# Kernel optimization log

Measured on AMD Instinct MI355X. Metric: run time of the kernel, lower is better.

Reference implementation:

```python
import math
import jax, jax.numpy as jnp
import numpy as np

B, T_IN, R = 32, 24, 512
T_HIST, WIDTH, MODES, NLAYERS = 24, 128, 64, 4
IN_CH = T_HIST + 4
STEPS = 12
DT = 1.0


def setup_inputs() -> dict:
    key = jax.random.key(0)
    ks = jax.random.split(key, 12)
    scale = 1.0 / math.sqrt(WIDTH * WIDTH)
    return {
        "z": jax.random.normal(ks[0], (B, T_IN, R), dtype=jnp.float32),
        "t_grid": jax.random.uniform(ks[1], (B, T_IN), dtype=jnp.float32) * 100.0,
        "fc0_w": jax.random.normal(ks[2], (IN_CH, WIDTH), dtype=jnp.float32) / math.sqrt(IN_CH),
        "fc0_b": jax.random.normal(ks[3], (WIDTH,), dtype=jnp.float32) * 0.01,
        "spec_wr": jax.random.normal(ks[4], (NLAYERS, WIDTH, WIDTH, MODES), dtype=jnp.float32) * scale,
        "spec_wi": jax.random.normal(ks[5], (NLAYERS, WIDTH, WIDTH, MODES), dtype=jnp.float32) * scale,
        "conv_w": jax.random.normal(ks[6], (NLAYERS, WIDTH, WIDTH), dtype=jnp.float32) / math.sqrt(WIDTH),
        "conv_b": jax.random.normal(ks[7], (NLAYERS, WIDTH), dtype=jnp.float32) * 0.01,
        "fc1_w": jax.random.normal(ks[8], (WIDTH, 2 * WIDTH), dtype=jnp.float32) / math.sqrt(WIDTH),
        "fc1_b": jax.random.normal(ks[9], (2 * WIDTH,), dtype=jnp.float32) * 0.01,
        "fc2_w": jax.random.normal(ks[10], (2 * WIDTH, 1), dtype=jnp.float32) / math.sqrt(2 * WIDTH),
        "fc2_b": jax.random.normal(ks[11], (1,), dtype=jnp.float32) * 0.01,
        "steps": STEPS,
    }


def _fno_block(h, w_cplx, cw, cb, r):
    # h: (B, W, R). Spectral conv: rfft -> truncated complex mul -> irfft.
    x_ft = jnp.fft.rfft(h, axis=-1)                      # (B, W, R//2+1) complex
    m = w_cplx.shape[-1]                                  # modes (<= R//2+1)
    out_m = jnp.einsum('bim,iom->bom', x_ft[:, :, :m], w_cplx)
    out_ft = jnp.pad(out_m, ((0, 0), (0, 0), (0, x_ft.shape[-1] - m)))
    spec = jnp.fft.irfft(out_ft, n=r, axis=-1)
    # 1x1 conv (pointwise over channels) + bias
    pw = jnp.einsum('oi,bir->bor', cw, h) + cb[None, :, None]
    return jax.nn.gelu(spec + pw, approximate=False)


def reference(z, t_grid, fc0_w, fc0_b, spec_wr, spec_wi, conv_w, conv_b,
              fc1_w, fc1_b, fc2_w, fc2_b, steps):
    b, _, r = z.shape
    t_hist = fc0_w.shape[0] - 4
    seq0 = z[:, -t_hist:]                 # (B, t_hist, R)
    t_start = t_grid[:, -1]               # (B,)
    x_coord = jnp.linspace(0.0, 1.0, r, dtype=z.dtype)  # (R,)
    spec_w = spec_wr + 1j * spec_wi       # (L, W, W, M) complex
    nlayers = conv_w.shape[0]

    def step(seq, i):
        tt = t_start + (i + 1).astype(z.dtype) * DT      # (B,)
        ang24 = 2.0 * math.pi * tt / 24.0
        ang168 = 2.0 * math.pi * tt / 168.0
        tf = jnp.stack([
            jnp.broadcast_to(jnp.sin(ang24)[:, None], (b, r)),
            jnp.broadcast_to(jnp.cos(ang24)[:, None], (b, r)),
            jnp.broadcast_to(jnp.sin(ang168)[:, None], (b, r)),
            jnp.broadcast_to(x_coord[None, :], (b, r)),
        ], axis=-1)                                       # (B, R, 4)
        h = jnp.concatenate([jnp.swapaxes(seq, 1, 2), tf], axis=-1)  # (B, R, t_hist+4)
        h = h @ fc0_w + fc0_b                             # (B, R, W)
        h = jnp.swapaxes(h, 1, 2)                         # (B, W, R)
        for l in range(nlayers):
            h = _fno_block(h, spec_w[l], conv_w[l], conv_b[l], r)
        h = jnp.swapaxes(h, 1, 2)                         # (B, R, W)
        h = jax.nn.gelu(h @ fc1_w + fc1_b, approximate=False)
        dx = (h @ fc2_w + fc2_b)[..., 0]                  # (B, R)
        z_next = seq[:, -1, :] + dx
        new_seq = jnp.concatenate([seq[:, 1:], z_next[:, None]], axis=1)
        return new_seq, z_next

    _, preds = jax.lax.scan(step, seq0, jnp.arange(steps))
    return jnp.swapaxes(preds, 0, 1)                      # (B, steps, R)
```

## Files before the change

kernel.cpp:

```cpp
#include <hip/hip_runtime.h>
#include <math.h>


#define NB 32
#define NR 512
#define NW 128
#define NM 64
#define NTH 24
#define NLAY 4
#define NSTEPS 12
#define SEQROWS 36

typedef unsigned short u16;
typedef unsigned int u32;
typedef __attribute__((ext_vector_type(8))) short bf16x8;
typedef __attribute__((ext_vector_type(4))) float f32x4;
#define MFMA16(a, b, c) __builtin_amdgcn_mfma_f32_16x16x32_bf16((a), (b), (c), 0, 0, 0)

__device__ __forceinline__ float gelu_exact(float x) {
    return 0.5f * x * (1.0f + erff(x * 0.70710678118654752f));
}
__device__ __forceinline__ float bf2f(u16 u) {
    union { u32 i; float f; } v; v.i = ((u32)u) << 16; return v.f;
}
__device__ __forceinline__ u16 f2bf_hi(float x) {
    union { float f; u32 i; } v; v.f = x; return (u16)(v.i >> 16);
}
__device__ __forceinline__ u16 f2bf_lo(float x) {
    float h = bf2f(f2bf_hi(x));
    return f2bf_hi(x - h);
}
__device__ __forceinline__ bf16x8 negbf(bf16x8 a) {
#pragma unroll
    for (int i = 0; i < 8; i++) a[i] ^= (short)0x8000;
    return a;
}

__global__ void build_tables_planes(u16* __restrict__ f1, u16* __restrict__ f2,
                                    u16* __restrict__ gt1, u16* __restrict__ gt2) {
    int idx = blockIdx.x * 256 + threadIdx.x;
    int mc = idx >> 9, r = idx & 511, m = mc & 63;
    int p = (m * r) & 511;
    float a = (float)p * (1.0f / 256.0f);
    float c = cospif(a), s = sinpif(a);
    float Fv = (mc < 64) ? c : -s;
    float cm = (m == 0) ? (1.0f / 512.0f) : (2.0f / 512.0f);
    float Gv = (mc < 64) ? cm * c : ((m == 0) ? 0.0f : -cm * s);
    f1[idx] = f2bf_hi(Fv); f2[idx] = f2bf_lo(Fv);
    size_t g = (size_t)r * 128 + mc;
    gt1[g] = f2bf_hi(Gv); gt2[g] = f2bf_lo(Gv);
}

__global__ __launch_bounds__(256) void prep_specw(const float* __restrict__ wr, const float* __restrict__ wi,
                           u16* __restrict__ wr1, u16* __restrict__ wr2,
                           u16* __restrict__ wi1, u16* __restrict__ wi2) {
    __shared__ float tile[128][65];
    int l = blockIdx.x >> 7, o = blockIdx.x & 127;
    int tid = threadIdx.x;
    size_t sbase = (size_t)l * 1048576 + (size_t)o * 64;
    size_t dbase = (size_t)l * 64 * 16384 + (size_t)o * 128;
    for (int pass = 0; pass < 2; pass++) {
        const float* src = pass ? wi : wr;
        u16* d1 = pass ? wi1 : wr1;
        u16* d2 = pass ? wi2 : wr2;
        if (pass) __syncthreads();
        for (int e = tid; e < 8192; e += 256) {
            int i = e >> 6, m = e & 63;
            tile[i][m] = src[sbase + (size_t)i * 8192 + m];
        }
        __syncthreads();
        for (int e = tid; e < 4096; e += 256) {
            int m = e >> 6, i2 = (e & 63) * 2;
            float v0 = tile[i2][m], v1 = tile[i2 + 1][m];
            u32 hh = (u32)f2bf_hi(v0) | ((u32)f2bf_hi(v1) << 16);
            u32 ll = (u32)f2bf_lo(v0) | ((u32)f2bf_lo(v1) << 16);
            size_t d = dbase + (size_t)m * 16384 + i2;
            *(u32*)&d1[d] = hh;
            *(u32*)&d2[d] = ll;
        }
    }
}

__global__ void prep_cw(const float* __restrict__ cw, u16* __restrict__ c1, u16* __restrict__ c2) {
    int idx = blockIdx.x * 256 + threadIdx.x;
    float v = cw[idx];
    c1[idx] = f2bf_hi(v); c2[idx] = f2bf_lo(v);
}

__global__ void prep_fc1t(const float* __restrict__ fc1_w,
                          u16* __restrict__ f11, u16* __restrict__ f12) {
    int idx = blockIdx.x * 256 + threadIdx.x;
    int j = idx >> 7, c = idx & 127;
    float v = fc1_w[(size_t)c * 256 + j];
    f11[idx] = f2bf_hi(v); f12[idx] = f2bf_lo(v);
}

__global__ void init_seq_kernel(const float* __restrict__ z, float* __restrict__ seq) {
    int idx = blockIdx.x * 256 + threadIdx.x;
    int b = idx / (NTH * NR);
    int rem = idx - b * (NTH * NR);
    seq[(size_t)b * SEQROWS * NR + rem] = z[idx];
}

__global__ __launch_bounds__(256) void fc0_kernel(const float* __restrict__ seq,
        const float* __restrict__ t_grid, const float* __restrict__ fc0_w,
        const float* __restrict__ fc0_b, u16* __restrict__ ht1, u16* __restrict__ ht2,
        u16* __restrict__ htc1, u16* __restrict__ htc2, int step) {
    __shared__ float wlds[28 * 128];
    __shared__ float blds[128];
    int b = blockIdx.y, rblk = blockIdx.x;
    int tid = threadIdx.x;
    for (int t = tid; t < 28 * 128; t += 256) wlds[t] = fc0_w[t];
    if (tid < 128) blds[tid] = fc0_b[tid];
    __syncthreads();
    int lane = tid & 63, wq = tid >> 6;
    int r = rblk * 64 + lane;
    float sv[24];
    const float* sp = seq + ((size_t)b * SEQROWS + step) * NR + r;
#pragma unroll
    for (int t = 0; t < 24; t++) sv[t] = sp[(size_t)t * NR];
    float tt = t_grid[b * 24 + 23] + (float)(step + 1);
    float ang24 = 6.28318530717958647692f * tt * (1.0f / 24.0f);
    float ang168 = 6.28318530717958647692f * tt * (1.0f / 168.0f);
    float s24 = sinf(ang24), c24 = cosf(ang24), s168 = sinf(ang168);
    float xc = (float)r * (1.0f / 511.0f);
    size_t rowoff = ((size_t)b * NR + r) * NW;
#pragma unroll 2
    for (int w0 = 0; w0 < 32; w0 += 2) {
        float acc2[2];
#pragma unroll
        for (int q = 0; q < 2; q++) {
            int w = wq * 32 + w0 + q;
            float acc = blds[w];
#pragma unroll
            for (int t = 0; t < 24; t++) acc += sv[t] * wlds[t * 128 + w];
            acc += s24 * wlds[24 * 128 + w] + c24 * wlds[25 * 128 + w]
                 + s168 * wlds[26 * 128 + w] + xc * wlds[27 * 128 + w];
            acc2[q] = acc;
        }
        u16 h0 = f2bf_hi(acc2[0]), h1 = f2bf_hi(acc2[1]);
        u16 l0 = f2bf_lo(acc2[0]), l1 = f2bf_lo(acc2[1]);
        size_t off = rowoff + wq * 32 + w0;
        *(u32*)&ht1[off] = (u32)h0 | ((u32)h1 << 16);
        *(u32*)&ht2[off] = (u32)l0 | ((u32)l1 << 16);
        int w = wq * 32 + w0;
        size_t coff = ((size_t)b * 128 + w) * 512 + r;
        htc1[coff] = h0; htc1[coff + 512] = h1;
        htc2[coff] = l0; htc2[coff + 512] = l1;
    }
}

__global__ __launch_bounds__(256) void dft_mfma(const u16* __restrict__ f1, const u16* __restrict__ f2,
        const u16* __restrict__ htc1, const u16* __restrict__ htc2,
        u16* __restrict__ x1, u16* __restrict__ x2) {
    __shared__ __align__(16) u16 A1[2][32 * 72], A2[2][32 * 72];
    __shared__ __align__(16) u16 B1[2][32 * 72], B2[2][32 * 72];
    int bx = blockIdx.x;
    int mct = blockIdx.y * 32;
    int tid = threadIdx.x, wid = tid >> 6, l = tid & 63;
    int wm0 = (wid >> 1) * 16, wn0 = (wid & 1) * 16;
    int arow = l & 15, kgrp = (l >> 4) * 8;
    f32x4 acc = {0.f, 0.f, 0.f, 0.f};
    int pl = tid >> 7, row = (tid >> 2) & 31, sp = (tid & 3) * 16;
    const u16* asrc = (pl ? f2 : f1) + (size_t)(mct + row) * 512 + sp;
    const u16* bsrc = (pl ? htc2 : htc1)
                      + ((size_t)(bx >> 2) * 128 + (bx & 3) * 32 + row) * 512 + sp;
    int loff = row * 72 + sp;
    u16* ad0 = (pl ? A2[0] : A1[0]) + loff;  u16* ad1 = (pl ? A2[1] : A1[1]) + loff;
    u16* bd0 = (pl ? B2[0] : B1[0]) + loff;  u16* bd1 = (pl ? B2[1] : B1[1]) + loff;
    uint4 oA0, oA1, oB0, oB1, eA0, eA1, eB0, eB1;
    oA0 = *(const uint4*)(asrc);     oA1 = *(const uint4*)(asrc + 8);
    oB0 = *(const uint4*)(bsrc);     oB1 = *(const uint4*)(bsrc + 8);
    *(uint4*)ad0 = oA0; *(uint4*)(ad0 + 8) = oA1;
    *(uint4*)bd0 = oB0; *(uint4*)(bd0 + 8) = oB1;
    oA0 = *(const uint4*)(asrc + 64);  oA1 = *(const uint4*)(asrc + 72);
    oB0 = *(const uint4*)(bsrc + 64);  oB1 = *(const uint4*)(bsrc + 72);
    eA0 = *(const uint4*)(asrc + 128); eA1 = *(const uint4*)(asrc + 136);
    eB0 = *(const uint4*)(bsrc + 128); eB1 = *(const uint4*)(bsrc + 136);
    __syncthreads();
#define DFT_COMPUTE(BUF)                                                       \
    { _Pragma("unroll")                                                        \
      for (int kk = 0; kk < 64; kk += 32) {                                    \
        bf16x8 a1 = *(const bf16x8*)&A1[BUF][(wm0 + arow) * 72 + kk + kgrp];   \
        bf16x8 a2 = *(const bf16x8*)&A2[BUF][(wm0 + arow) * 72 + kk + kgrp];   \
        bf16x8 b1 = *(const bf16x8*)&B1[BUF][(wn0 + arow) * 72 + kk + kgrp];   \
        bf16x8 b2 = *(const bf16x8*)&B2[BUF][(wn0 + arow) * 72 + kk + kgrp];   \
        acc = MFMA16(a1, b1, acc);                                             \
        acc = MFMA16(a1, b2, acc);                                             \
        acc = MFMA16(a2, b1, acc);                                             \
      } }
    for (int k = 0; k < 8; k += 2) {
        DFT_COMPUTE(0)
        *(uint4*)ad1 = oA0; *(uint4*)(ad1 + 8) = oA1;
        *(uint4*)bd1 = oB0; *(uint4*)(bd1 + 8) = oB1;
        if (k < 5) {
            int ko = (k + 3) * 64;
            oA0 = *(const uint4*)(asrc + ko);      oA1 = *(const uint4*)(asrc + ko + 8);
            oB0 = *(const uint4*)(bsrc + ko);      oB1 = *(const uint4*)(bsrc + ko + 8);
        }
        __syncthreads();
        DFT_COMPUTE(1)
        if (k < 6) {
            *(uint4*)ad0 = eA0; *(uint4*)(ad0 + 8) = eA1;
            *(uint4*)bd0 = eB0; *(uint4*)(bd0 + 8) = eB1;
            if (k < 4) {
                int ko = (k + 4) * 64;
                eA0 = *(const uint4*)(asrc + ko);  eA1 = *(const uint4*)(asrc + ko + 8);
                eB0 = *(const uint4*)(bsrc + ko);  eB1 = *(const uint4*)(bsrc + ko + 8);
            }
        }
        __syncthreads();
    }
#undef DFT_COMPUTE
    int mcr = mct + wm0 + (l >> 4) * 4;
    int n0 = bx * 32 + wn0 + (l & 15);
#pragma unroll
    for (int j = 0; j < 4; j++) {
        size_t o0 = (size_t)(mcr + j) * 4096 + n0;
        x1[o0] = f2bf_hi(acc[j]); x2[o0] = f2bf_lo(acc[j]);
    }
}

__global__ __launch_bounds__(256) void modemix_mfma(const u16* __restrict__ x1, const u16* __restrict__ x2,
        const u16* __restrict__ wr1, const u16* __restrict__ wr2,
        const u16* __restrict__ wi1, const u16* __restrict__ wi2,
        u16* __restrict__ y1, u16* __restrict__ y2, int layer) {
    __shared__ __align__(16) u16 POOL[8 * 32 * 136];
    int m = blockIdx.x, oq = blockIdx.y;
    int tid = threadIdx.x, wid = tid >> 6, l = tid & 63;
    int wo0 = (wid >> 1) * 16, wb0 = (wid & 1) * 16;
    int arow = l & 15, kgrp = (l >> 4) * 8;
    size_t wbase = (((size_t)layer * 64 + m) * 128 + oq * 32) * 128;
#pragma unroll
    for (int q = 0; q < 16; q++) {
        const int slab = q >> 1;
        int rr = ((q & 1) << 4) + (tid >> 4);
        int seg = tid & 15;
        const u16* src;
        if      (slab == 0) src = wr1 + wbase + (size_t)rr * 128 + seg * 8;
        else if (slab == 1) src = wr2 + wbase + (size_t)rr * 128 + seg * 8;
        else if (slab == 2) src = wi1 + wbase + (size_t)rr * 128 + seg * 8;
        else if (slab == 3) src = wi2 + wbase + (size_t)rr * 128 + seg * 8;
        else if (slab == 4) src = x1 + (size_t)m * 4096 + rr * 128 + seg * 8;
        else if (slab == 5) src = x2 + (size_t)m * 4096 + rr * 128 + seg * 8;
        else if (slab == 6) src = x1 + (size_t)(64 + m) * 4096 + rr * 128 + seg * 8;
        else                src = x2 + (size_t)(64 + m) * 4096 + rr * 128 + seg * 8;
        *(uint4*)&POOL[slab * 4352 + rr * 136 + seg * 8] = *(const uint4*)src;
    }
    __syncthreads();
    f32x4 ar = {0.f, 0.f, 0.f, 0.f}, ai = {0.f, 0.f, 0.f, 0.f};
    int aoB = (wo0 + arow) * 136 + kgrp;
    int boB = (wb0 + arow) * 136 + kgrp;
#pragma unroll
    for (int kg = 0; kg < 4; kg++) {
        int ao = aoB + kg * 32;
        int bo = boB + kg * 32;
        bf16x8 Wr1 = *(const bf16x8*)&POOL[0 * 4352 + ao];
        bf16x8 Wr2 = *(const bf16x8*)&POOL[1 * 4352 + ao];
        bf16x8 Wi1 = *(const bf16x8*)&POOL[2 * 4352 + ao];
        bf16x8 Wi2 = *(const bf16x8*)&POOL[3 * 4352 + ao];
        bf16x8 Xr1 = *(const bf16x8*)&POOL[4 * 4352 + bo];
        bf16x8 Xr2 = *(const bf16x8*)&POOL[5 * 4352 + bo];
        bf16x8 Xi1 = *(const bf16x8*)&POOL[6 * 4352 + bo];
        bf16x8 Xi2 = *(const bf16x8*)&POOL[7 * 4352 + bo];
        bf16x8 nWi1 = negbf(Wi1), nWi2 = negbf(Wi2);
        ar = MFMA16(Wr1, Xr1, ar); ar = MFMA16(Wr1, Xr2, ar); ar = MFMA16(Wr2, Xr1, ar);
        ar = MFMA16(nWi1, Xi1, ar); ar = MFMA16(nWi1, Xi2, ar); ar = MFMA16(nWi2, Xi1, ar);
        ai = MFMA16(Wi1, Xr1, ai); ai = MFMA16(Wi1, Xr2, ai); ai = MFMA16(Wi2, Xr1, ai);
        ai = MFMA16(Wr1, Xi1, ai); ai = MFMA16(Wr1, Xi2, ai); ai = MFMA16(Wr2, Xi1, ai);
    }
    int ob = oq * 32 + wo0 + (l >> 4) * 4;
    int bb = wb0 + (l & 15);
#pragma unroll
    for (int j = 0; j < 4; j++) {
        size_t o = ((size_t)bb * 128 + ob + j) * 128;
        y1[o + m] = f2bf_hi(ar[j]); y2[o + m] = f2bf_lo(ar[j]);
        y1[o + 64 + m] = f2bf_hi(ai[j]); y2[o + 64 + m] = f2bf_lo(ai[j]);
    }
}

__global__ __launch_bounds__(256) void idft_conv_mfma(const u16* __restrict__ y1, const u16* __restrict__ y2,
        const u16* __restrict__ gt1, const u16* __restrict__ gt2,
        const u16* __restrict__ hc1, const u16* __restrict__ hc2,
        const u16* __restrict__ cw1, const u16* __restrict__ cw2,
        const float* __restrict__ conv_b,
        u16* __restrict__ hn1, u16* __restrict__ hn2,
        u16* __restrict__ htc1, u16* __restrict__ htc2, int layer, int wtr) {
    __shared__ __align__(16) u16 A1[2][2560], A2[2][2560];
    __shared__ __align__(16) u16 B1[2][2560], B2[2][2560];
    __shared__ __align__(16) u16 T1[64 * 66], T2[64 * 66];
    int rt = blockIdx.x * 64, ot = blockIdx.y * 64, b = blockIdx.z;
    int tid = threadIdx.x, wid = tid >> 6, l = tid & 63;
    int wo0 = (wid >> 1) * 32, wr0 = (wid & 1) * 32;
    int arow = (l & 15), kgrp = (l >> 4) * 8;
    int srow = (tid >> 2) & 63, sseg = tid & 3;
    int soff = srow * 40 + sseg * 8;
    const u16* ya = y1 + ((size_t)b * 128 + ot + srow) * 128 + sseg * 8;
    const u16* yb = y2 + ((size_t)b * 128 + ot + srow) * 128 + sseg * 8;
    const u16* ca = cw1 + ((size_t)layer * 128 + ot + srow) * 128 + sseg * 8;
    const u16* cb = cw2 + ((size_t)layer * 128 + ot + srow) * 128 + sseg * 8;
    const u16* ga = gt1 + (size_t)(rt + srow) * 128 + sseg * 8;
    const u16* gb = gt2 + (size_t)(rt + srow) * 128 + sseg * 8;
    const u16* ha = hc1 + ((size_t)b * 512 + rt + srow) * 128 + sseg * 8;
    const u16* hb = hc2 + ((size_t)b * 512 + rt + srow) * 128 + sseg * 8;
    f32x4 acc[2][2] = {{{0.f,0.f,0.f,0.f},{0.f,0.f,0.f,0.f}},{{0.f,0.f,0.f,0.f},{0.f,0.f,0.f,0.f}}};
    uint4 raO0, raO1, rbO0, rbO1, raE0, raE1, rbE0, rbE1;
#define IDFT_LOAD(chk, Ra0, Ra1, Rb0, Rb1)                                    \
    {   int k0_ = ((chk) & 3) * 32;                                           \
        if ((chk) < 4) {                                                      \
            Ra0 = *(const uint4*)(ya + k0_); Ra1 = *(const uint4*)(yb + k0_); \
            Rb0 = *(const uint4*)(ga + k0_); Rb1 = *(const uint4*)(gb + k0_); \
        } else {                                                              \
            Ra0 = *(const uint4*)(ca + k0_); Ra1 = *(const uint4*)(cb + k0_); \
            Rb0 = *(const uint4*)(ha + k0_); Rb1 = *(const uint4*)(hb + k0_); \
        } }
#define IDFT_STORE(BUF, Ra0, Ra1, Rb0, Rb1)                                   \
    {   *(uint4*)(A1[BUF] + soff) = Ra0; *(uint4*)(A2[BUF] + soff) = Ra1;     \
        *(uint4*)(B1[BUF] + soff) = Rb0; *(uint4*)(B2[BUF] + soff) = Rb1; }
#define IDFT_COMPUTE(BUF)                                                     \
    {   bf16x8 bfr[2][2];                                                     \
        _Pragma("unroll")                                                     \
        for (int rf = 0; rf < 2; rf++) {                                      \
            bfr[rf][0] = *(const bf16x8*)&B1[BUF][(wr0 + rf * 16 + arow) * 40 + kgrp]; \
            bfr[rf][1] = *(const bf16x8*)&B2[BUF][(wr0 + rf * 16 + arow) * 40 + kgrp]; \
        }                                                                     \
        _Pragma("unroll")                                                     \
        for (int of = 0; of < 2; of++) {                                      \
            bf16x8 a1 = *(const bf16x8*)&A1[BUF][(wo0 + of * 16 + arow) * 40 + kgrp]; \
            bf16x8 a2 = *(const bf16x8*)&A2[BUF][(wo0 + of * 16 + arow) * 40 + kgrp]; \
            _Pragma("unroll")                                                 \
            for (int rf = 0; rf < 2; rf++) {                                  \
                acc[of][rf] = MFMA16(a1, bfr[rf][0], acc[of][rf]);            \
                acc[of][rf] = MFMA16(a1, bfr[rf][1], acc[of][rf]);            \
                acc[of][rf] = MFMA16(a2, bfr[rf][0], acc[of][rf]);            \
            }                                                                 \
        } }
    IDFT_LOAD(0, raO0, raO1, rbO0, rbO1)
    IDFT_STORE(0, raO0, raO1, rbO0, rbO1)
    IDFT_LOAD(1, raO0, raO1, rbO0, rbO1)
    IDFT_LOAD(2, raE0, raE1, rbE0, rbE1)
    __syncthreads();
    for (int k = 0; k < 8; k += 2) {
        IDFT_COMPUTE(0)
        IDFT_STORE(1, raO0, raO1, rbO0, rbO1)
        if (k < 5) IDFT_LOAD(k + 3, raO0, raO1, rbO0, rbO1)
        __syncthreads();
        IDFT_COMPUTE(1)
        if (k < 6) {
            IDFT_STORE(0, raE0, raE1, rbE0, rbE1)
            if (k < 4) IDFT_LOAD(k + 4, raE0, raE1, rbE0, rbE1)
        }
        __syncthreads();
    }
#undef IDFT_LOAD
#undef IDFT_STORE
#undef IDFT_COMPUTE
#pragma unroll
    for (int of = 0; of < 2; of++) {
        int obl = wo0 + of * 16 + (l >> 4) * 4;
        int ob = ot + obl;
#pragma unroll
        for (int rf = 0; rf < 2; rf++) {
            int rloc = wr0 + rf * 16 + (l & 15);
            int r = rt + rloc;
            float v0 = gelu_exact(acc[of][rf][0] + conv_b[layer * 128 + ob + 0]);
            float v1 = gelu_exact(acc[of][rf][1] + conv_b[layer * 128 + ob + 1]);
            float v2 = gelu_exact(acc[of][rf][2] + conv_b[layer * 128 + ob + 2]);
            float v3 = gelu_exact(acc[of][rf][3] + conv_b[layer * 128 + ob + 3]);
            ushort4 hv, lv;
            hv.x = f2bf_hi(v0); hv.y = f2bf_hi(v1); hv.z = f2bf_hi(v2); hv.w = f2bf_hi(v3);
            lv.x = f2bf_lo(v0); lv.y = f2bf_lo(v1); lv.z = f2bf_lo(v2); lv.w = f2bf_lo(v3);
            size_t off = ((size_t)b * 512 + r) * 128 + ob;
            *(ushort4*)&hn1[off] = hv;
            *(ushort4*)&hn2[off] = lv;
            if (wtr) {
                T1[(obl + 0) * 66 + rloc] = hv.x; T1[(obl + 1) * 66 + rloc] = hv.y;
                T1[(obl + 2) * 66 + rloc] = hv.z; T1[(obl + 3) * 66 + rloc] = hv.w;
                T2[(obl + 0) * 66 + rloc] = lv.x; T2[(obl + 1) * 66 + rloc] = lv.y;
                T2[(obl + 2) * 66 + rloc] = lv.z; T2[(obl + 3) * 66 + rloc] = lv.w;
            }
        }
    }
    if (wtr) {
        __syncthreads();
#pragma unroll
        for (int q = 0; q < 8; q++) {
            int t = tid + q * 256;
            int o = t >> 5, ru = t & 31;
            u32 vh = *(const u32*)&T1[o * 66 + ru * 2];
            u32 vl = *(const u32*)&T2[o * 66 + ru * 2];
            size_t off = ((size_t)b * 128 + ot + o) * 512 + rt + ru * 2;
            *(u32*)&htc1[off] = vh;
            *(u32*)&htc2[off] = vl;
        }
    }
}

__global__ __launch_bounds__(256) void head_mfma(const u16* __restrict__ ht1, const u16* __restrict__ ht2,
        const u16* __restrict__ f11, const u16* __restrict__ f12,
        const float* __restrict__ fc1_b, const float* __restrict__ fc2_w,
        const float* __restrict__ fc2_b,
        const float* __restrict__ t_grid, const float* __restrict__ fc0_w,
        const float* __restrict__ fc0_b,
        float* __restrict__ seq, float* __restrict__ preds,
        u16* __restrict__ nht1, u16* __restrict__ nht2,
        u16* __restrict__ nhtc1, u16* __restrict__ nhtc2,
        int step, int do_fc0) {
    __shared__ __align__(16) u16 POOL[25600];
    __shared__ float fc2s[256], fc1bs[256];
    u16* HA1 = POOL;
    u16* HA2 = POOL + 10240;
    u16* HB1 = POOL + 20480;
    u16* HB2 = POOL + 23040;
    int blk = blockIdx.x;
    int b = blk >> 3, r0 = (blk & 7) * 64;
    int tid = threadIdx.x, wid = tid >> 6, l = tid & 63;
    fc2s[tid] = fc2_w[tid];
    fc1bs[tid] = fc1_b[tid];
    int arow = l & 15, kgrp = (l >> 4) * 8;
    f32x4 acc[16];
#pragma unroll
    for (int jf = 0; jf < 16; jf++) acc[jf] = (f32x4){0.f, 0.f, 0.f, 0.f};
    for (int k0 = 0; k0 < 128; k0 += 32) {
        __syncthreads();
#pragma unroll
        for (int q = 0; q < 8; q++) {
            int t = tid + q * 256;
            int pl = t >> 10, j = (t >> 2) & 255, seg = t & 3;
            const u16* src = (pl ? f12 : f11) + (size_t)j * 128 + k0 + seg * 8;
            *(uint4*)((pl ? HA2 : HA1) + j * 40 + seg * 8) = *(const uint4*)src;
        }
#pragma unroll
        for (int q = 0; q < 2; q++) {
            int t = tid + q * 256;
            int pl = t >> 8, rr = (t >> 2) & 63, seg = t & 3;
            const u16* src = (pl ? ht2 : ht1) + ((size_t)b * 512 + r0 + rr) * 128 + k0 + seg * 8;
            *(uint4*)((pl ? HB2 : HB1) + rr * 40 + seg * 8) = *(const uint4*)src;
        }
        __syncthreads();
        int bo = (wid * 16 + arow) * 40 + kgrp;
        bf16x8 b1 = *(const bf16x8*)&HB1[bo];
        bf16x8 b2 = *(const bf16x8*)&HB2[bo];
#pragma unroll
        for (int jf = 0; jf < 16; jf++) {
            int ao = (jf * 16 + arow) * 40 + kgrp;
            bf16x8 a1 = *(const bf16x8*)&HA1[ao];
            bf16x8 a2 = *(const bf16x8*)&HA2[ao];
            acc[jf] = MFMA16(a1, b1, acc[jf]);
            acc[jf] = MFMA16(a1, b2, acc[jf]);
            acc[jf] = MFMA16(a2, b1, acc[jf]);
        }
    }
    __syncthreads();
    float dx = 0.0f;
#pragma unroll
    for (int jf = 0; jf < 16; jf++) {
        int jbase = jf * 16 + (l >> 4) * 4;
#pragma unroll
        for (int jj = 0; jj < 4; jj++) {
            int j = jbase + jj;
            dx += gelu_exact(acc[jf][jj] + fc1bs[j]) * fc2s[j];
        }
    }
    dx += __shfl_xor(dx, 16);
    dx += __shfl_xor(dx, 32);
    bool zlane = ((l >> 4) == 0);
    int rml = wid * 16 + arow;
    float zn = 0.0f;
    if (zlane) {
        int r = r0 + rml;
        zn = seq[((size_t)b * SEQROWS + step + 23) * NR + r] + dx + fc2_b[0];
        seq[((size_t)b * SEQROWS + step + 24) * NR + r] = zn;
        preds[((size_t)b * NSTEPS + step) * NR + r] = zn;
    }
    if (!do_fc0) return;
    float* win = (float*)POOL;
    float* wl  = (float*)POOL + 2048;
    float* bl  = (float*)POOL + 2048 + 3584;
    for (int t = tid; t < 23 * 64; t += 256) {
        int tr = t >> 6, c = t & 63;
        win[tr * 64 + c] = seq[((size_t)b * SEQROWS + step + 1 + tr) * NR + r0 + c];
    }
    for (int t = tid; t < 28 * 128; t += 256) wl[t] = fc0_w[t];
    if (tid < 128) bl[tid] = fc0_b[tid];
    if (zlane) win[23 * 64 + rml] = zn;
    __syncthreads();
    int lane = tid & 63, wq = tid >> 6;
    int r = r0 + lane;
    float sv[24];
#pragma unroll
    for (int t = 0; t < 24; t++) sv[t] = win[t * 64 + lane];
    float tt = t_grid[b * 24 + 23] + (float)(step + 2);
    float ang24 = 6.28318530717958647692f * tt * (1.0f / 24.0f);
    float ang168 = 6.28318530717958647692f * tt * (1.0f / 168.0f);
    float s24 = sinf(ang24), c24 = cosf(ang24), s168 = sinf(ang168);
    float xc = (float)r * (1.0f / 511.0f);
    size_t rowoff = ((size_t)b * NR + r) * NW;
#pragma unroll 2
    for (int w0 = 0; w0 < 32; w0 += 2) {
        float acc2[2];
#pragma unroll
        for (int q = 0; q < 2; q++) {
            int w = wq * 32 + w0 + q;
            float a = bl[w];
#pragma unroll
            for (int t = 0; t < 24; t++) a += sv[t] * wl[t * 128 + w];
            a += s24 * wl[24 * 128 + w] + c24 * wl[25 * 128 + w]
               + s168 * wl[26 * 128 + w] + xc * wl[27 * 128 + w];
            acc2[q] = a;
        }
        u16 h0 = f2bf_hi(acc2[0]), h1 = f2bf_hi(acc2[1]);
        u16 l0 = f2bf_lo(acc2[0]), l1 = f2bf_lo(acc2[1]);
        size_t off = rowoff + wq * 32 + w0;
        *(u32*)&nht1[off] = (u32)h0 | ((u32)h1 << 16);
        *(u32*)&nht2[off] = (u32)l0 | ((u32)l1 << 16);
        int w = wq * 32 + w0;
        size_t coff = ((size_t)b * 128 + w) * 512 + r;
        nhtc1[coff] = h0; nhtc1[coff + 512] = h1;
        nhtc2[coff] = l0; nhtc2[coff + 512] = l1;
    }
}

extern "C" void kernel_launch(void* const* d_in, const int* in_sizes, int n_in,
                              void* d_out, int out_size, void* d_ws, size_t ws_size,
                              hipStream_t stream) {
    (void)in_sizes; (void)n_in; (void)out_size; (void)ws_size;
    const float* z       = (const float*)d_in[0];
    const float* t_grid  = (const float*)d_in[1];
    const float* fc0_w   = (const float*)d_in[2];
    const float* fc0_b   = (const float*)d_in[3];
    const float* spec_wr = (const float*)d_in[4];
    const float* spec_wi = (const float*)d_in[5];
    const float* conv_w  = (const float*)d_in[6];
    const float* conv_b  = (const float*)d_in[7];
    const float* fc1_w   = (const float*)d_in[8];
    const float* fc1_b   = (const float*)d_in[9];
    const float* fc2_w   = (const float*)d_in[10];
    const float* fc2_b   = (const float*)d_in[11];
    float* preds = (float*)d_out;

    char* p = (char*)d_ws;
    float* seq = (float*)p;  p += (size_t)NB * SEQROWS * NR * 4;
    u16* ht1 = (u16*)p;  p += (size_t)2 * NB * NR * NW * 2;
    u16* ht2 = (u16*)p;  p += (size_t)2 * NB * NR * NW * 2;
    u16* htc1 = (u16*)p; p += (size_t)NB * NW * NR * 2;
    u16* htc2 = (u16*)p; p += (size_t)NB * NW * NR * 2;
    u16* x1  = (u16*)p;  p += (size_t)128 * 4096 * 2;
    u16* x2  = (u16*)p;  p += (size_t)128 * 4096 * 2;
    u16* y1  = (u16*)p;  p += (size_t)NB * NW * 128 * 2;
    u16* y2  = (u16*)p;  p += (size_t)NB * NW * 128 * 2;
    u16* f1  = (u16*)p;  p += (size_t)128 * 512 * 2;
    u16* f2  = (u16*)p;  p += (size_t)128 * 512 * 2;
    u16* gt1 = (u16*)p;  p += (size_t)512 * 128 * 2;
    u16* gt2 = (u16*)p;  p += (size_t)512 * 128 * 2;
    u16* wr1 = (u16*)p;  p += (size_t)NLAY * NM * NW * NW * 2;
    u16* wr2 = (u16*)p;  p += (size_t)NLAY * NM * NW * NW * 2;
    u16* wi1 = (u16*)p;  p += (size_t)NLAY * NM * NW * NW * 2;
    u16* wi2 = (u16*)p;  p += (size_t)NLAY * NM * NW * NW * 2;
    u16* cw1 = (u16*)p;  p += (size_t)NLAY * NW * NW * 2;
    u16* cw2 = (u16*)p;  p += (size_t)NLAY * NW * NW * 2;
    u16* f11 = (u16*)p;  p += (size_t)256 * 128 * 2;
    u16* f12 = (u16*)p;  p += (size_t)256 * 128 * 2;

    const size_t htplane = (size_t)NB * NR * NW;

    build_tables_planes<<<256, 256, 0, stream>>>(f1, f2, gt1, gt2);
    prep_specw<<<512, 256, 0, stream>>>(spec_wr, spec_wi, wr1, wr2, wi1, wi2);
    prep_cw<<<256, 256, 0, stream>>>(conv_w, cw1, cw2);
    prep_fc1t<<<128, 256, 0, stream>>>(fc1_w, f11, f12);
    init_seq_kernel<<<(NB * NTH * NR) / 256, 256, 0, stream>>>(z, seq);

    for (int step = 0; step < NSTEPS; step++) {
        if (step == 0) {
            fc0_kernel<<<dim3(8, 32), 256, 0, stream>>>(seq, t_grid, fc0_w, fc0_b,
                                                        ht1, ht2, htc1, htc2, step);
        }
        int cur = 0;
        for (int l = 0; l < NLAY; l++) {
            const u16* hc1 = ht1 + (size_t)cur * htplane;
            const u16* hc2 = ht2 + (size_t)cur * htplane;
            u16* hn1 = ht1 + (size_t)(cur ^ 1) * htplane;
            u16* hn2 = ht2 + (size_t)(cur ^ 1) * htplane;
            dft_mfma<<<dim3(128, 4), 256, 0, stream>>>(f1, f2, htc1, htc2, x1, x2);
            modemix_mfma<<<dim3(64, 4), 256, 0, stream>>>(x1, x2, wr1, wr2, wi1, wi2,
                                                          y1, y2, l);
            idft_conv_mfma<<<dim3(8, 2, 32), 256, 0, stream>>>(y1, y2, gt1, gt2,
                                                               hc1, hc2, cw1, cw2,
                                                               conv_b, hn1, hn2,
                                                               htc1, htc2, l, (l < 3) ? 1 : 0);
            cur ^= 1;
        }
        head_mfma<<<256, 256, 0, stream>>>(ht1, ht2, f11, f12, fc1_b, fc2_w, fc2_b,
                                           t_grid, fc0_w, fc0_b, seq, preds,
                                           ht1, ht2, htc1, htc2,
                                           step, (step < NSTEPS - 1) ? 1 : 0);
    }
}
```

Before: 1.810 ms.

## Fuse last-layer inverse DFT/conv with head MLP and merge setup kernels

```diff
diff --git a/kernel.cpp b/kernel.cpp
--- a/kernel.cpp
+++ b/kernel.cpp
@@ -36,19 +36,40 @@
     return a;
 }
 
-__global__ void build_tables_planes(u16* __restrict__ f1, u16* __restrict__ f2,
-                                    u16* __restrict__ gt1, u16* __restrict__ gt2) {
+__global__ void setup_misc(const float* __restrict__ z, const float* __restrict__ conv_w,
+                           const float* __restrict__ fc1_w,
+                           u16* __restrict__ f1, u16* __restrict__ f2,
+                           u16* __restrict__ gt1, u16* __restrict__ gt2,
+                           u16* __restrict__ cw1, u16* __restrict__ cw2,
+                           u16* __restrict__ f11, u16* __restrict__ f12,
+                           float* __restrict__ seq) {
     int idx = blockIdx.x * 256 + threadIdx.x;
-    int mc = idx >> 9, r = idx & 511, m = mc & 63;
-    int p = (m * r) & 511;
-    float a = (float)p * (1.0f / 256.0f);
-    float c = cospif(a), s = sinpif(a);
-    float Fv = (mc < 64) ? c : -s;
-    float cm = (m == 0) ? (1.0f / 512.0f) : (2.0f / 512.0f);
-    float Gv = (mc < 64) ? cm * c : ((m == 0) ? 0.0f : -cm * s);
-    f1[idx] = f2bf_hi(Fv); f2[idx] = f2bf_lo(Fv);
-    size_t g = (size_t)r * 128 + mc;
-    gt1[g] = f2bf_hi(Gv); gt2[g] = f2bf_lo(Gv);
+    if (idx < 65536) {
+        int mc = idx >> 9, r = idx & 511, m = mc & 63;
+        int p = (m * r) & 511;
+        float a = (float)p * (1.0f / 256.0f);
+        float c = cospif(a), s = sinpif(a);
+        float Fv = (mc < 64) ? c : -s;
+        float cm = (m == 0) ? (1.0f / 512.0f) : (2.0f / 512.0f);
+        float Gv = (mc < 64) ? cm * c : ((m == 0) ? 0.0f : -cm * s);
+        f1[idx] = f2bf_hi(Fv); f2[idx] = f2bf_lo(Fv);
+        size_t g = (size_t)r * 128 + mc;
+        gt1[g] = f2bf_hi(Gv); gt2[g] = f2bf_lo(Gv);
+    } else if (idx < 131072) {
+        int i = idx - 65536;
+        float v = conv_w[i];
+        cw1[i] = f2bf_hi(v); cw2[i] = f2bf_lo(v);
+    } else if (idx < 163840) {
+        int i = idx - 131072;
+        int j = i >> 7, c = i & 127;
+        float v = fc1_w[(size_t)c * 256 + j];
+        f11[i] = f2bf_hi(v); f12[i] = f2bf_lo(v);
+    } else {
+        int i = idx - 163840;
+        int b = i / (NTH * NR);
+        int rem = i - b * (NTH * NR);
+        seq[(size_t)b * SEQROWS * NR + rem] = z[i];
+    }
 }
 
 __global__ __launch_bounds__(256) void prep_specw(const float* __restrict__ wr, const float* __restrict__ wi,
@@ -79,27 +100,6 @@
             *(u32*)&d2[d] = ll;
         }
     }
-}
-
-__global__ void prep_cw(const float* __restrict__ cw, u16* __restrict__ c1, u16* __restrict__ c2) {
-    int idx = blockIdx.x * 256 + threadIdx.x;
-    float v = cw[idx];
-    c1[idx] = f2bf_hi(v); c2[idx] = f2bf_lo(v);
-}
-
-__global__ void prep_fc1t(const float* __restrict__ fc1_w,
-                          u16* __restrict__ f11, u16* __restrict__ f12) {
-    int idx = blockIdx.x * 256 + threadIdx.x;
-    int j = idx >> 7, c = idx & 127;
-    float v = fc1_w[(size_t)c * 256 + j];
-    f11[idx] = f2bf_hi(v); f12[idx] = f2bf_lo(v);
-}
-
-__global__ void init_seq_kernel(const float* __restrict__ z, float* __restrict__ seq) {
-    int idx = blockIdx.x * 256 + threadIdx.x;
-    int b = idx / (NTH * NR);
-    int rem = idx - b * (NTH * NR);
-    seq[(size_t)b * SEQROWS * NR + rem] = z[idx];
 }
 
 __global__ __launch_bounds__(256) void fc0_kernel(const float* __restrict__ seq,
@@ -285,7 +285,7 @@
         const u16* __restrict__ cw1, const u16* __restrict__ cw2,
         const float* __restrict__ conv_b,
         u16* __restrict__ hn1, u16* __restrict__ hn2,
-        u16* __restrict__ htc1, u16* __restrict__ htc2, int layer, int wtr) {
+        u16* __restrict__ htc1, u16* __restrict__ htc2, int layer) {
     __shared__ __align__(16) u16 A1[2][2560], A2[2][2560];
     __shared__ __align__(16) u16 B1[2][2560], B2[2][2560];
     __shared__ __align__(16) u16 T1[64 * 66], T2[64 * 66];
@@ -305,7 +305,7 @@
     const u16* hb = hc2 + ((size_t)b * 512 + rt + srow) * 128 + sseg * 8;
     f32x4 acc[2][2] = {{{0.f,0.f,0.f,0.f},{0.f,0.f,0.f,0.f}},{{0.f,0.f,0.f,0.f},{0.f,0.f,0.f,0.f}}};
     uint4 raO0, raO1, rbO0, rbO1, raE0, raE1, rbE0, rbE1;
-#define IDFT_LOAD(chk, Ra0, Ra1, Rb0, Rb1)                                    \
+#define ILOAD(chk, Ra0, Ra1, Rb0, Rb1)                                        \
     {   int k0_ = ((chk) & 3) * 32;                                           \
         if ((chk) < 4) {                                                      \
             Ra0 = *(const uint4*)(ya + k0_); Ra1 = *(const uint4*)(yb + k0_); \
@@ -314,10 +314,10 @@
             Ra0 = *(const uint4*)(ca + k0_); Ra1 = *(const uint4*)(cb + k0_); \
             Rb0 = *(const uint4*)(ha + k0_); Rb1 = *(const uint4*)(hb + k0_); \
         } }
-#define IDFT_STORE(BUF, Ra0, Ra1, Rb0, Rb1)                                   \
+#define ISTORE(BUF, Ra0, Ra1, Rb0, Rb1)                                      \
     {   *(uint4*)(A1[BUF] + soff) = Ra0; *(uint4*)(A2[BUF] + soff) = Ra1;     \
         *(uint4*)(B1[BUF] + soff) = Rb0; *(uint4*)(B2[BUF] + soff) = Rb1; }
-#define IDFT_COMPUTE(BUF)                                                     \
+#define ICOMP(BUF)                                                            \
     {   bf16x8 bfr[2][2];                                                     \
         _Pragma("unroll")                                                     \
         for (int rf = 0; rf < 2; rf++) {                                      \
@@ -335,26 +335,26 @@
                 acc[of][rf] = MFMA16(a2, bfr[rf][0], acc[of][rf]);            \
             }                                                                 \
         } }
-    IDFT_LOAD(0, raO0, raO1, rbO0, rbO1)
-    IDFT_STORE(0, raO0, raO1, rbO0, rbO1)
-    IDFT_LOAD(1, raO0, raO1, rbO0, rbO1)
-    IDFT_LOAD(2, raE0, raE1, rbE0, rbE1)
+    ILOAD(0, raO0, raO1, rbO0, rbO1)
+    ISTORE(0, raO0, raO1, rbO0, rbO1)
+    ILOAD(1, raO0, raO1, rbO0, rbO1)
+    ILOAD(2, raE0, raE1, rbE0, rbE1)
     __syncthreads();
     for (int k = 0; k < 8; k += 2) {
-        IDFT_COMPUTE(0)
-        IDFT_STORE(1, raO0, raO1, rbO0, rbO1)
-        if (k < 5) IDFT_LOAD(k + 3, raO0, raO1, rbO0, rbO1)
-        __syncthreads();
-        IDFT_COMPUTE(1)
+        ICOMP(0)
+        ISTORE(1, raO0, raO1, rbO0, rbO1)
+        if (k < 5) ILOAD(k + 3, raO0, raO1, rbO0, rbO1)
+        __syncthreads();
+        ICOMP(1)
         if (k < 6) {
-            IDFT_STORE(0, raE0, raE1, rbE0, rbE1)
-            if (k < 4) IDFT_LOAD(k + 4, raE0, raE1, rbE0, rbE1)
-        }
-        __syncthreads();
-    }
-#undef IDFT_LOAD
-#undef IDFT_STORE
-#undef IDFT_COMPUTE
+            ISTORE(0, raE0, raE1, rbE0, rbE1)
+            if (k < 4) ILOAD(k + 4, raE0, raE1, rbE0, rbE1)
+        }
+        __syncthreads();
+    }
+#undef ILOAD
+#undef ISTORE
+#undef ICOMP
 #pragma unroll
     for (int of = 0; of < 2; of++) {
         int obl = wo0 + of * 16 + (l >> 4) * 4;
@@ -373,30 +373,31 @@
             size_t off = ((size_t)b * 512 + r) * 128 + ob;
             *(ushort4*)&hn1[off] = hv;
             *(ushort4*)&hn2[off] = lv;
-            if (wtr) {
-                T1[(obl + 0) * 66 + rloc] = hv.x; T1[(obl + 1) * 66 + rloc] = hv.y;
-                T1[(obl + 2) * 66 + rloc] = hv.z; T1[(obl + 3) * 66 + rloc] = hv.w;
-                T2[(obl + 0) * 66 + rloc] = lv.x; T2[(obl + 1) * 66 + rloc] = lv.y;
-                T2[(obl + 2) * 66 + rloc] = lv.z; T2[(obl + 3) * 66 + rloc] = lv.w;
-            }
-        }
-    }
-    if (wtr) {
-        __syncthreads();
-#pragma unroll
-        for (int q = 0; q < 8; q++) {
-            int t = tid + q * 256;
-            int o = t >> 5, ru = t & 31;
-            u32 vh = *(const u32*)&T1[o * 66 + ru * 2];
-            u32 vl = *(const u32*)&T2[o * 66 + ru * 2];
-            size_t off = ((size_t)b * 128 + ot + o) * 512 + rt + ru * 2;
-            *(u32*)&htc1[off] = vh;
-            *(u32*)&htc2[off] = vl;
-        }
-    }
-}
-
-__global__ __launch_bounds__(256) void head_mfma(const u16* __restrict__ ht1, const u16* __restrict__ ht2,
+            T1[(obl + 0) * 66 + rloc] = hv.x; T1[(obl + 1) * 66 + rloc] = hv.y;
+            T1[(obl + 2) * 66 + rloc] = hv.z; T1[(obl + 3) * 66 + rloc] = hv.w;
+            T2[(obl + 0) * 66 + rloc] = lv.x; T2[(obl + 1) * 66 + rloc] = lv.y;
+            T2[(obl + 2) * 66 + rloc] = lv.z; T2[(obl + 3) * 66 + rloc] = lv.w;
+        }
+    }
+    __syncthreads();
+#pragma unroll
+    for (int q = 0; q < 8; q++) {
+        int t = tid + q * 256;
+        int o = t >> 5, ru = t & 31;
+        u32 vh = *(const u32*)&T1[o * 66 + ru * 2];
+        u32 vl = *(const u32*)&T2[o * 66 + ru * 2];
+        size_t off = ((size_t)b * 128 + ot + o) * 512 + rt + ru * 2;
+        *(u32*)&htc1[off] = vh;
+        *(u32*)&htc2[off] = vl;
+    }
+}
+
+__global__ __launch_bounds__(256) void idft_head_mfma(
+        const u16* __restrict__ y1, const u16* __restrict__ y2,
+        const u16* __restrict__ gt1, const u16* __restrict__ gt2,
+        const u16* __restrict__ hc1, const u16* __restrict__ hc2,
+        const u16* __restrict__ cw1, const u16* __restrict__ cw2,
+        const float* __restrict__ conv_b,
         const u16* __restrict__ f11, const u16* __restrict__ f12,
         const float* __restrict__ fc1_b, const float* __restrict__ fc2_w,
         const float* __restrict__ fc2_b,
@@ -405,61 +406,162 @@
         float* __restrict__ seq, float* __restrict__ preds,
         u16* __restrict__ nht1, u16* __restrict__ nht2,
         u16* __restrict__ nhtc1, u16* __restrict__ nhtc2,
-        int step, int do_fc0) {
-    __shared__ __align__(16) u16 POOL[25600];
-    __shared__ float fc2s[256], fc1bs[256];
-    u16* HA1 = POOL;
-    u16* HA2 = POOL + 10240;
-    u16* HB1 = POOL + 20480;
-    u16* HB2 = POOL + 23040;
-    int blk = blockIdx.x;
-    int b = blk >> 3, r0 = (blk & 7) * 64;
+        int layer, int step, int do_fc0) {
+    __shared__ __align__(16) u16 POOL[35072];
+    int rt = blockIdx.x * 64, b = blockIdx.y;
     int tid = threadIdx.x, wid = tid >> 6, l = tid & 63;
+    int wo0 = (wid >> 1) * 32, wr0 = (wid & 1) * 32;
+    int arow = (l & 15), kgrp = (l >> 4) * 8;
+    u16* A1 = POOL;
+    u16* A2 = POOL + 10240;
+    u16* B1 = POOL + 20480;
+    u16* B2 = POOL + 25600;
+    int srow = tid >> 2, sseg = tid & 3;
+    const u16* ya0 = y1 + ((size_t)b * 128 + srow) * 128 + sseg * 8;
+    const u16* ya1 = ya0 + 64 * 128;
+    const u16* yb0 = y2 + ((size_t)b * 128 + srow) * 128 + sseg * 8;
+    const u16* yb1 = yb0 + 64 * 128;
+    const u16* ca0 = cw1 + ((size_t)layer * 128 + srow) * 128 + sseg * 8;
+    const u16* ca1 = ca0 + 64 * 128;
+    const u16* cb0 = cw2 + ((size_t)layer * 128 + srow) * 128 + sseg * 8;
+    const u16* cb1 = cb0 + 64 * 128;
+    const u16* ga = gt1 + (size_t)(rt + srow) * 128 + sseg * 8;
+    const u16* gb = gt2 + (size_t)(rt + srow) * 128 + sseg * 8;
+    const u16* ha = hc1 + ((size_t)b * 512 + rt + srow) * 128 + sseg * 8;
+    const u16* hb = hc2 + ((size_t)b * 512 + rt + srow) * 128 + sseg * 8;
+    int soffA0 = srow * 40 + sseg * 8;
+    int soffA1 = (srow + 64) * 40 + sseg * 8;
+    f32x4 acc[2][2][2];
+#pragma unroll
+    for (int ot = 0; ot < 2; ot++)
+#pragma unroll
+        for (int of = 0; of < 2; of++)
+#pragma unroll
+            for (int rf = 0; rf < 2; rf++) acc[ot][of][rf] = (f32x4){0.f, 0.f, 0.f, 0.f};
+    uint4 oA0, oA1r, oA2r, oA3, oB0, oB1;
+    uint4 eA0, eA1r, eA2r, eA3, eB0, eB1;
+#define ILOAD(chk, Q0, Q1, Q2, Q3, R0, R1)                                    \
+    {   int k0_ = ((chk) & 3) * 32;                                           \
+        if ((chk) < 4) {                                                      \
+            Q0 = *(const uint4*)(ya0 + k0_); Q1 = *(const uint4*)(ya1 + k0_); \
+            Q2 = *(const uint4*)(yb0 + k0_); Q3 = *(const uint4*)(yb1 + k0_); \
+            R0 = *(const uint4*)(ga + k0_);  R1 = *(const uint4*)(gb + k0_);  \
+        } else {                                                              \
+            Q0 = *(const uint4*)(ca0 + k0_); Q1 = *(const uint4*)(ca1 + k0_); \
+            Q2 = *(const uint4*)(cb0 + k0_); Q3 = *(const uint4*)(cb1 + k0_); \
+            R0 = *(const uint4*)(ha + k0_);  R1 = *(const uint4*)(hb + k0_);  \
+        } }
+#define ISTORE(BUF, Q0, Q1, Q2, Q3, R0, R1)                                   \
+    {   *(uint4*)(A1 + (BUF) * 5120 + soffA0) = Q0;                           \
+        *(uint4*)(A1 + (BUF) * 5120 + soffA1) = Q1;                           \
+        *(uint4*)(A2 + (BUF) * 5120 + soffA0) = Q2;                           \
+        *(uint4*)(A2 + (BUF) * 5120 + soffA1) = Q3;                           \
+        *(uint4*)(B1 + (BUF) * 2560 + soffA0) = R0;                           \
+        *(uint4*)(B2 + (BUF) * 2560 + soffA0) = R1; }
+#define ICOMP(BUF)                                                            \
+    {   bf16x8 bfr[2][2];                                                     \
+        _Pragma("unroll")                                                     \
+        for (int rf = 0; rf < 2; rf++) {                                      \
+            bfr[rf][0] = *(const bf16x8*)&B1[(BUF) * 2560 + (wr0 + rf * 16 + arow) * 40 + kgrp]; \
+            bfr[rf][1] = *(const bf16x8*)&B2[(BUF) * 2560 + (wr0 + rf * 16 + arow) * 40 + kgrp]; \
+        }                                                                     \
+        _Pragma("unroll")                                                     \
+        for (int ot = 0; ot < 2; ot++) {                                      \
+        _Pragma("unroll")                                                     \
+        for (int of = 0; of < 2; of++) {                                      \
+            bf16x8 a1v = *(const bf16x8*)&A1[(BUF) * 5120 + (ot * 64 + wo0 + of * 16 + arow) * 40 + kgrp]; \
+            bf16x8 a2v = *(const bf16x8*)&A2[(BUF) * 5120 + (ot * 64 + wo0 + of * 16 + arow) * 40 + kgrp]; \
+            _Pragma("unroll")                                                 \
+            for (int rf = 0; rf < 2; rf++) {                                  \
+                acc[ot][of][rf] = MFMA16(a1v, bfr[rf][0], acc[ot][of][rf]);   \
+                acc[ot][of][rf] = MFMA16(a1v, bfr[rf][1], acc[ot][of][rf]);   \
+                acc[ot][of][rf] = MFMA16(a2v, bfr[rf][0], acc[ot][of][rf]);   \
+            }                                                                 \
+        } } }
+    ILOAD(0, oA0, oA1r, oA2r, oA3, oB0, oB1)
+    ISTORE(0, oA0, oA1r, oA2r, oA3, oB0, oB1)
+    ILOAD(1, oA0, oA1r, oA2r, oA3, oB0, oB1)
+    ILOAD(2, eA0, eA1r, eA2r, eA3, eB0, eB1)
+    __syncthreads();
+    for (int k = 0; k < 8; k += 2) {
+        ICOMP(0)
+        ISTORE(1, oA0, oA1r, oA2r, oA3, oB0, oB1)
+        if (k < 5) ILOAD(k + 3, oA0, oA1r, oA2r, oA3, oB0, oB1)
+        __syncthreads();
+        ICOMP(1)
+        if (k < 6) {
+            ISTORE(0, eA0, eA1r, eA2r, eA3, eB0, eB1)
+            if (k < 4) ILOAD(k + 4, eA0, eA1r, eA2r, eA3, eB0, eB1)
+        }
+        __syncthreads();
+    }
+#undef ILOAD
+#undef ISTORE
+#undef ICOMP
+    __syncthreads();
+    u16* h1 = POOL;
+    u16* h2 = POOL + 8704;
+#pragma unroll
+    for (int ot = 0; ot < 2; ot++) {
+#pragma unroll
+        for (int of = 0; of < 2; of++) {
+            int obl = ot * 64 + wo0 + of * 16 + (l >> 4) * 4;
+#pragma unroll
+            for (int rf = 0; rf < 2; rf++) {
+                int rloc = wr0 + rf * 16 + (l & 15);
+                float v0 = gelu_exact(acc[ot][of][rf][0] + conv_b[layer * 128 + obl + 0]);
+                float v1 = gelu_exact(acc[ot][of][rf][1] + conv_b[layer * 128 + obl + 1]);
+                float v2 = gelu_exact(acc[ot][of][rf][2] + conv_b[layer * 128 + obl + 2]);
+                float v3 = gelu_exact(acc[ot][of][rf][3] + conv_b[layer * 128 + obl + 3]);
+                ushort4 hv, lv;
+                hv.x = f2bf_hi(v0); hv.y = f2bf_hi(v1); hv.z = f2bf_hi(v2); hv.w = f2bf_hi(v3);
+                lv.x = f2bf_lo(v0); lv.y = f2bf_lo(v1); lv.z = f2bf_lo(v2); lv.w = f2bf_lo(v3);
+                *(ushort4*)&h1[rloc * 136 + obl] = hv;
+                *(ushort4*)&h2[rloc * 136 + obl] = lv;
+            }
+        }
+    }
+    u16* HA1 = POOL + 17408;
+    u16* HA2 = POOL + 22528;
+    float* fc2s = (float*)(POOL + 27648);
+    float* fc1bs = (float*)(POOL + 28160);
     fc2s[tid] = fc2_w[tid];
     fc1bs[tid] = fc1_b[tid];
-    int arow = l & 15, kgrp = (l >> 4) * 8;
-    f32x4 acc[16];
-#pragma unroll
-    for (int jf = 0; jf < 16; jf++) acc[jf] = (f32x4){0.f, 0.f, 0.f, 0.f};
-    for (int k0 = 0; k0 < 128; k0 += 32) {
-        __syncthreads();
-#pragma unroll
-        for (int q = 0; q < 8; q++) {
-            int t = tid + q * 256;
-            int pl = t >> 10, j = (t >> 2) & 255, seg = t & 3;
-            const u16* src = (pl ? f12 : f11) + (size_t)j * 128 + k0 + seg * 8;
-            *(uint4*)((pl ? HA2 : HA1) + j * 40 + seg * 8) = *(const uint4*)src;
-        }
-#pragma unroll
-        for (int q = 0; q < 2; q++) {
-            int t = tid + q * 256;
-            int pl = t >> 8, rr = (t >> 2) & 63, seg = t & 3;
-            const u16* src = (pl ? ht2 : ht1) + ((size_t)b * 512 + r0 + rr) * 128 + k0 + seg * 8;
-            *(uint4*)((pl ? HB2 : HB1) + rr * 40 + seg * 8) = *(const uint4*)src;
-        }
-        __syncthreads();
-        int bo = (wid * 16 + arow) * 40 + kgrp;
-        bf16x8 b1 = *(const bf16x8*)&HB1[bo];
-        bf16x8 b2 = *(const bf16x8*)&HB2[bo];
-#pragma unroll
-        for (int jf = 0; jf < 16; jf++) {
-            int ao = (jf * 16 + arow) * 40 + kgrp;
-            bf16x8 a1 = *(const bf16x8*)&HA1[ao];
-            bf16x8 a2 = *(const bf16x8*)&HA2[ao];
-            acc[jf] = MFMA16(a1, b1, acc[jf]);
-            acc[jf] = MFMA16(a1, b2, acc[jf]);
-            acc[jf] = MFMA16(a2, b1, acc[jf]);
-        }
-    }
-    __syncthreads();
     float dx = 0.0f;
-#pragma unroll
-    for (int jf = 0; jf < 16; jf++) {
-        int jbase = jf * 16 + (l >> 4) * 4;
-#pragma unroll
-        for (int jj = 0; jj < 4; jj++) {
-            int j = jbase + jj;
-            dx += gelu_exact(acc[jf][jj] + fc1bs[j]) * fc2s[j];
+    for (int jh = 0; jh < 2; jh++) {
+        f32x4 hacc[8];
+#pragma unroll
+        for (int jf = 0; jf < 8; jf++) hacc[jf] = (f32x4){0.f, 0.f, 0.f, 0.f};
+        for (int k0 = 0; k0 < 128; k0 += 32) {
+            __syncthreads();
+#pragma unroll
+            for (int q = 0; q < 4; q++) {
+                int t = tid + q * 256;
+                int pl = t >> 9, j = (t >> 2) & 127, seg = t & 3;
+                const u16* src = (pl ? f12 : f11) + (size_t)(jh * 128 + j) * 128 + k0 + seg * 8;
+                *(uint4*)((pl ? HA2 : HA1) + j * 40 + seg * 8) = *(const uint4*)src;
+            }
+            __syncthreads();
+            int bo = (wid * 16 + arow) * 136 + k0 + kgrp;
+            bf16x8 hb1 = *(const bf16x8*)&h1[bo];
+            bf16x8 hb2 = *(const bf16x8*)&h2[bo];
+#pragma unroll
+            for (int jf = 0; jf < 8; jf++) {
+                int ao = (jf * 16 + arow) * 40 + kgrp;
+                bf16x8 a1 = *(const bf16x8*)&HA1[ao];
+                bf16x8 a2 = *(const bf16x8*)&HA2[ao];
+                hacc[jf] = MFMA16(a1, hb1, hacc[jf]);
+                hacc[jf] = MFMA16(a1, hb2, hacc[jf]);
+                hacc[jf] = MFMA16(a2, hb1, hacc[jf]);
+            }
+        }
+#pragma unroll
+        for (int jf = 0; jf < 8; jf++) {
+            int jbase = jh * 128 + jf * 16 + (l >> 4) * 4;
+#pragma unroll
+            for (int jj = 0; jj < 4; jj++) {
+                dx += gelu_exact(hacc[jf][jj] + fc1bs[jbase + jj]) * fc2s[jbase + jj];
+            }
         }
     }
     dx += __shfl_xor(dx, 16);
@@ -468,56 +570,58 @@
     int rml = wid * 16 + arow;
     float zn = 0.0f;
     if (zlane) {
-        int r = r0 + rml;
+        int r = rt + rml;
         zn = seq[((size_t)b * SEQROWS + step + 23) * NR + r] + dx + fc2_b[0];
         seq[((size_t)b * SEQROWS + step + 24) * NR + r] = zn;
         preds[((size_t)b * NSTEPS + step) * NR + r] = zn;
     }
-    if (!do_fc0) return;
-    float* win = (float*)POOL;
-    float* wl  = (float*)POOL + 2048;
-    float* bl  = (float*)POOL + 2048 + 3584;
-    for (int t = tid; t < 23 * 64; t += 256) {
-        int tr = t >> 6, c = t & 63;
-        win[tr * 64 + c] = seq[((size_t)b * SEQROWS + step + 1 + tr) * NR + r0 + c];
-    }
-    for (int t = tid; t < 28 * 128; t += 256) wl[t] = fc0_w[t];
-    if (tid < 128) bl[tid] = fc0_b[tid];
-    if (zlane) win[23 * 64 + rml] = zn;
-    __syncthreads();
-    int lane = tid & 63, wq = tid >> 6;
-    int r = r0 + lane;
-    float sv[24];
-#pragma unroll
-    for (int t = 0; t < 24; t++) sv[t] = win[t * 64 + lane];
-    float tt = t_grid[b * 24 + 23] + (float)(step + 2);
-    float ang24 = 6.28318530717958647692f * tt * (1.0f / 24.0f);
-    float ang168 = 6.28318530717958647692f * tt * (1.0f / 168.0f);
-    float s24 = sinf(ang24), c24 = cosf(ang24), s168 = sinf(ang168);
-    float xc = (float)r * (1.0f / 511.0f);
-    size_t rowoff = ((size_t)b * NR + r) * NW;
+    if (do_fc0) {
+        float* win = (float*)POOL;
+        float* wl  = (float*)POOL + 2048;
+        float* bl  = (float*)POOL + 2048 + 3584;
+        __syncthreads();
+        for (int t = tid; t < 23 * 64; t += 256) {
+            int tr = t >> 6, c = t & 63;
+            win[tr * 64 + c] = seq[((size_t)b * SEQROWS + step + 1 + tr) * NR + rt + c];
+        }
+        for (int t = tid; t < 28 * 128; t += 256) wl[t] = fc0_w[t];
+        if (tid < 128) bl[tid] = fc0_b[tid];
+        if (zlane) win[23 * 64 + rml] = zn;
+        __syncthreads();
+        int lane = tid & 63, wq = tid >> 6;
+        int r = rt + lane;
+        float sv[24];
+#pragma unroll
+        for (int t = 0; t < 24; t++) sv[t] = win[t * 64 + lane];
+        float tt = t_grid[b * 24 + 23] + (float)(step + 2);
+        float ang24 = 6.28318530717958647692f * tt * (1.0f / 24.0f);
+        float ang168 = 6.28318530717958647692f * tt * (1.0f / 168.0f);
+        float s24 = sinf(ang24), c24 = cosf(ang24), s168 = sinf(ang168);
+        float xc = (float)r * (1.0f / 511.0f);
+        size_t rowoff = ((size_t)b * NR + r) * NW;
 #pragma unroll 2
-    for (int w0 = 0; w0 < 32; w0 += 2) {
-        float acc2[2];
-#pragma unroll
-        for (int q = 0; q < 2; q++) {
-            int w = wq * 32 + w0 + q;
-            float a = bl[w];
-#pragma unroll
-            for (int t = 0; t < 24; t++) a += sv[t] * wl[t * 128 + w];
-            a += s24 * wl[24 * 128 + w] + c24 * wl[25 * 128 + w]
-               + s168 * wl[26 * 128 + w] + xc * wl[27 * 128 + w];
-            acc2[q] = a;
-        }
-        u16 h0 = f2bf_hi(acc2[0]), h1 = f2bf_hi(acc2[1]);
-        u16 l0 = f2bf_lo(acc2[0]), l1 = f2bf_lo(acc2[1]);
-        size_t off = rowoff + wq * 32 + w0;
-        *(u32*)&nht1[off] = (u32)h0 | ((u32)h1 << 16);
-        *(u32*)&nht2[off] = (u32)l0 | ((u32)l1 << 16);
-        int w = wq * 32 + w0;
-        size_t coff = ((size_t)b * 128 + w) * 512 + r;
-        nhtc1[coff] = h0; nhtc1[coff + 512] = h1;
-        nhtc2[coff] = l0; nhtc2[coff + 512] = l1;
+        for (int w0 = 0; w0 < 32; w0 += 2) {
+            float acc2[2];
+#pragma unroll
+            for (int q = 0; q < 2; q++) {
+                int w = wq * 32 + w0 + q;
+                float a = bl[w];
+#pragma unroll
+                for (int t = 0; t < 24; t++) a += sv[t] * wl[t * 128 + w];
+                a += s24 * wl[24 * 128 + w] + c24 * wl[25 * 128 + w]
+                   + s168 * wl[26 * 128 + w] + xc * wl[27 * 128 + w];
+                acc2[q] = a;
+            }
+            u16 h0 = f2bf_hi(acc2[0]), h1v = f2bf_hi(acc2[1]);
+            u16 l0 = f2bf_lo(acc2[0]), l1v = f2bf_lo(acc2[1]);
+            size_t off = rowoff + wq * 32 + w0;
+            *(u32*)&nht1[off] = (u32)h0 | ((u32)h1v << 16);
+            *(u32*)&nht2[off] = (u32)l0 | ((u32)l1v << 16);
+            int w = wq * 32 + w0;
+            size_t coff = ((size_t)b * 128 + w) * 512 + r;
+            nhtc1[coff] = h0; nhtc1[coff + 512] = h1v;
+            nhtc2[coff] = l0; nhtc2[coff + 512] = l1v;
+        }
     }
 }
 
@@ -564,17 +668,13 @@
 
     const size_t htplane = (size_t)NB * NR * NW;
 
-    build_tables_planes<<<256, 256, 0, stream>>>(f1, f2, gt1, gt2);
+    setup_misc<<<2176, 256, 0, stream>>>(z, conv_w, fc1_w, f1, f2, gt1, gt2,
+                                         cw1, cw2, f11, f12, seq);
     prep_specw<<<512, 256, 0, stream>>>(spec_wr, spec_wi, wr1, wr2, wi1, wi2);
-    prep_cw<<<256, 256, 0, stream>>>(conv_w, cw1, cw2);
-    prep_fc1t<<<128, 256, 0, stream>>>(fc1_w, f11, f12);
-    init_seq_kernel<<<(NB * NTH * NR) / 256, 256, 0, stream>>>(z, seq);
+    fc0_kernel<<<dim3(8, 32), 256, 0, stream>>>(seq, t_grid, fc0_w, fc0_b,
+                                                ht1, ht2, htc1, htc2, 0);
 
     for (int step = 0; step < NSTEPS; step++) {
-        if (step == 0) {
-            fc0_kernel<<<dim3(8, 32), 256, 0, stream>>>(seq, t_grid, fc0_w, fc0_b,
-                                                        ht1, ht2, htc1, htc2, step);
-        }
         int cur = 0;
         for (int l = 0; l < NLAY; l++) {
             const u16* hc1 = ht1 + (size_t)cur * htplane;
@@ -584,15 +684,19 @@
             dft_mfma<<<dim3(128, 4), 256, 0, stream>>>(f1, f2, htc1, htc2, x1, x2);
             modemix_mfma<<<dim3(64, 4), 256, 0, stream>>>(x1, x2, wr1, wr2, wi1, wi2,
                                                           y1, y2, l);
-            idft_conv_mfma<<<dim3(8, 2, 32), 256, 0, stream>>>(y1, y2, gt1, gt2,
-                                                               hc1, hc2, cw1, cw2,
-                                                               conv_b, hn1, hn2,
-                                                               htc1, htc2, l, (l < 3) ? 1 : 0);
+            if (l < 3) {
+                idft_conv_mfma<<<dim3(8, 2, 32), 256, 0, stream>>>(y1, y2, gt1, gt2,
+                                                                   hc1, hc2, cw1, cw2,
+                                                                   conv_b, hn1, hn2,
+                                                                   htc1, htc2, l);
+            } else {
+                idft_head_mfma<<<dim3(8, 32), 256, 0, stream>>>(
+                    y1, y2, gt1, gt2, hc1, hc2, cw1, cw2, conv_b,
+                    f11, f12, fc1_b, fc2_w, fc2_b, t_grid, fc0_w, fc0_b,
+                    seq, preds, ht1, ht2, htc1, htc2,
+                    l, step, (step < NSTEPS - 1) ? 1 : 0);
+            }
             cur ^= 1;
         }
-        head_mfma<<<256, 256, 0, stream>>>(ht1, ht2, f11, f12, fc1_b, fc2_w, fc2_b,
-                                           t_grid, fc0_w, fc0_b, seq, preds,
-                                           ht1, ht2, htc1, htc2,
-                                           step, (step < NSTEPS - 1) ? 1 : 0);
-    }
-}
+    }
+}
```

Measured after the change: 1.761 ms. -2.7%, faster.
